# Kernel optimization log

Hardware: AMD Instinct MI355X
Metric: run time of the kernel (lower is better)

## Reference

```python
import jax, jax.numpy as jnp
import numpy as np

B, NQ, NK = 4, 1024, 1536
DQ = DK = DV = 1024
DI = 4096
H = 16
EPS = 1e-5

def _ln(x, g, b):
    mu = jnp.mean(x, axis=-1, keepdims=True)
    var = jnp.mean((x - mu) ** 2, axis=-1, keepdims=True)
    return (x - mu) * jax.lax.rsqrt(var + EPS) * g + b

def setup_inputs() -> dict:
    key = jax.random.key(0)
    ks = jax.random.split(key, 20)
    s = 0.02
    inp = {
        "Q": jax.random.normal(ks[0], (B, NQ, DQ), jnp.float32),
        "K": jax.random.normal(ks[1], (B, NK, DK), jnp.float32),
        "knn_masks": jax.random.normal(ks[2], (B * H, NQ, 1024), jnp.float32),
        "mask_pos": 1024,
        "Wq": jax.random.normal(ks[3], (DQ, DV), jnp.float32) * s,
        "bq": jnp.zeros((DV,), jnp.float32),
        "Wk": jax.random.normal(ks[4], (DK, DV), jnp.float32) * s,
        "bk": jnp.zeros((DV,), jnp.float32),
        "Wv": jax.random.normal(ks[5], (DK, DV), jnp.float32) * s,
        "bv": jnp.zeros((DV,), jnp.float32),
        "Wo0": jax.random.normal(ks[6], (DV, DV), jnp.float32) * s,
        "bo0": jnp.zeros((DV,), jnp.float32),
        "Wo": jax.random.normal(ks[7], (DV, DI), jnp.float32) * s,
        "bo": jnp.zeros((DI,), jnp.float32),
        "Wo2": jax.random.normal(ks[8], (DI, DV), jnp.float32) * s,
        "bo2": jnp.zeros((DV,), jnp.float32),
        "g0": jnp.ones((DV,), jnp.float32),
        "beta0": jnp.zeros((DV,), jnp.float32),
        "g1": jnp.ones((DV,), jnp.float32),
        "beta1": jnp.zeros((DV,), jnp.float32),
    }
    return inp

def reference(Q, K, knn_masks, mask_pos, Wq, bq, Wk, bk, Wv, bv,
              Wo0, bo0, Wo, bo, Wo2, bo2, g0, beta0, g1, beta1):
    dh = DV // H
    q = Q @ Wq + bq                      # [B,NQ,DV]
    k = K @ Wk + bk                      # [B,NK,DV]
    v = K @ Wv + bv
    # torch cat(split(.,dh,2),0) -> head-major [H,B,N,dh]
    qh = q.reshape(B, NQ, H, dh).transpose(2, 0, 1, 3)
    kh = k[:, :mask_pos].reshape(B, mask_pos, H, dh).transpose(2, 0, 1, 3)
    vh = v[:, :mask_pos].reshape(B, mask_pos, H, dh).transpose(2, 0, 1, 3)
    logits = jnp.einsum("hbqd,hbkd->hbqk", qh, kh) / jnp.sqrt(jnp.float32(DV))
    logits = logits + knn_masks.reshape(H, B, NQ, mask_pos)
    attn = jax.nn.softmax(logits, axis=-1)
    o = jnp.einsum("hbqk,hbkd->hbqd", attn, vh)   # [H,B,NQ,dh]
    o = o.transpose(1, 2, 0, 3).reshape(B, NQ, DV)  # concat heads
    o = o @ Wo0 + bo0
    O = q + o
    O = _ln(O, g0, beta0)
    ff = jax.nn.relu(O @ Wo + bo) @ Wo2 + bo2
    O = O + ff
    O = _ln(O, g1, beta1)
    return O
```

## Files before the change

kernel.cpp:

```cpp
#include <hip/hip_runtime.h>
#include <hip/hip_bf16.h>

typedef unsigned short u16;
typedef __attribute__((ext_vector_type(4))) short bf16x4;
typedef __attribute__((ext_vector_type(8))) short bf16x8;
typedef __attribute__((ext_vector_type(4))) float f32x4;

static __device__ __forceinline__ u16 f2b(float f){
  union { float f; unsigned u; } v; v.f = f;
  unsigned r = v.u + 0x7fffu + ((v.u >> 16) & 1u);
  return (u16)(r >> 16);
}
static __device__ __forceinline__ float b2f(u16 h){
  union { unsigned u; float f; } v; v.u = ((unsigned)h) << 16; return v.f;
}
static __device__ __forceinline__ void gld_lds16(const void* g, void* l){
  __builtin_amdgcn_global_load_lds((const __attribute__((address_space(1))) void*)g,
                                   (__attribute__((address_space(3))) void*)l, 16, 0, 0);
}

__global__ __launch_bounds__(256) void prep(const float* __restrict__ Q,
                                            const float* __restrict__ K,
                                            u16* __restrict__ Qb, u16* __restrict__ Kb,
                                            const float* __restrict__ Wq, u16* __restrict__ Wq_t,
                                            const float* __restrict__ Wk, u16* __restrict__ Wk_t,
                                            const float* __restrict__ Wv, u16* __restrict__ Wv_t,
                                            const float* __restrict__ Wo0, u16* __restrict__ Wo0_t,
                                            const float* __restrict__ Wo, u16* __restrict__ Wo_t,
                                            const float* __restrict__ Wo2, u16* __restrict__ Wo2_t){
  __shared__ float tile[64][65];
  const int id = blockIdx.x, t = threadIdx.x;
  if (id < 8192){
    const float* src; u16* dst;
    if (id < 4096){
      src = Q + (size_t)id * 1024; dst = Qb + (size_t)id * 1024;
    } else {
      int r = id - 4096;
      size_t ir = (size_t)r + (size_t)(r >> 10) * 512;
      src = K + ir * 1024; dst = Kb + (size_t)r * 1024;
    }
    const float4 v = *(const float4*)(src + t * 4);
    bf16x4 o;
    o[0] = (short)f2b(v.x); o[1] = (short)f2b(v.y);
    o[2] = (short)f2b(v.z); o[3] = (short)f2b(v.w);
    *(bf16x4*)(dst + t * 4) = o;
    return;
  }
  int wid = id - 8192;
  const float* in; u16* out; int Kd, N, bx, by;
  if (wid < 1024){
    int sel = wid >> 8, local = wid & 255;
    bx = local & 15; by = local >> 4; Kd = 1024; N = 1024;
    in  = (sel == 0) ? Wq   : (sel == 1) ? Wk   : (sel == 2) ? Wv   : Wo0;
    out = (sel == 0) ? Wq_t : (sel == 1) ? Wk_t : (sel == 2) ? Wv_t : Wo0_t;
  } else if (wid < 2048){
    int local = wid - 1024; bx = local & 63; by = local >> 6; Kd = 1024; N = 4096;
    in = Wo; out = Wo_t;
  } else {
    int local = wid - 2048; bx = local & 15; by = local >> 4; Kd = 4096; N = 1024;
    in = Wo2; out = Wo2_t;
  }
  const int k0 = by * 64, n0 = bx * 64;
  const int tr = t >> 4, tc = t & 15;
#pragma unroll
  for (int i = 0; i < 4; i++){
    int r = tr + i * 16;
    float4 v = *(const float4*)(in + (size_t)(k0 + r) * N + n0 + tc * 4);
    tile[r][tc*4+0] = v.x; tile[r][tc*4+1] = v.y; tile[r][tc*4+2] = v.z; tile[r][tc*4+3] = v.w;
  }
  __syncthreads();
#pragma unroll
  for (int i = 0; i < 4; i++){
    int nr = tr + i * 16;
    bf16x4 pk;
#pragma unroll
    for (int j = 0; j < 4; j++) pk[j] = (short)f2b(tile[tc*4+j][nr]);
    *(bf16x4*)(out + (size_t)(n0 + nr) * Kd + k0 + tc * 4) = pk;
  }
}

static __device__ __forceinline__ void gemm_mainloop(const u16* __restrict__ A,
                                                     const u16* __restrict__ Bt,
                                                     int lda, int ldb, int kbeg, int kend,
                                                     int m0, int n0,
                                                     u16* lA, u16* lB, f32x4 acc[4][4]){
  const int t = threadIdx.x, w = t >> 6, l = t & 63;
  const int wr = w >> 1, wc = w & 1;
  const int lrow = l >> 3, lc8 = l & 7;
  const int c = l & 15, g = l >> 4;
  for (int k0 = kbeg; k0 < kend; k0 += 64){
#pragma unroll
    for (int i = 0; i < 4; i++){
      int ch = w * 4 + i;
      int r  = ch * 8 + lrow;
      gld_lds16(A  + (size_t)(m0 + r) * lda + k0 + lc8 * 8, lA + ch * 512);
      gld_lds16(Bt + (size_t)(n0 + r) * ldb + k0 + lc8 * 8, lB + ch * 512);
    }
    __syncthreads();
#pragma unroll
    for (int ks = 0; ks < 2; ks++){
      bf16x8 af[4], bfr[4];
#pragma unroll
      for (int mi = 0; mi < 4; mi++){
        int row = wr * 64 + mi * 16 + c;
        af[mi] = *(const bf16x8*)((const char*)lA + row * 128 + ks * 64 + g * 16);
      }
#pragma unroll
      for (int ni = 0; ni < 4; ni++){
        int row = wc * 64 + ni * 16 + c;
        bfr[ni] = *(const bf16x8*)((const char*)lB + row * 128 + ks * 64 + g * 16);
      }
#pragma unroll
      for (int mi = 0; mi < 4; mi++)
#pragma unroll
        for (int ni = 0; ni < 4; ni++)
          acc[mi][ni] = __builtin_amdgcn_mfma_f32_16x16x32_bf16(af[mi], bfr[ni], acc[mi][ni], 0, 0, 0);
    }
    __syncthreads();
  }
}

__global__ __launch_bounds__(256) void gemm_sk2(const u16* __restrict__ A,
                                                const u16* __restrict__ Bt,
                                                float* __restrict__ pout){
  __shared__ u16 lA[128 * 64];
  __shared__ u16 lB[128 * 64];
  const int t = threadIdx.x, w = t >> 6, l = t & 63;
  const int m0 = blockIdx.y * 128, n0 = blockIdx.x * 128;
  const int wr = w >> 1, wc = w & 1;
  const int c = l & 15, g = l >> 4;
  const int kbeg = blockIdx.z * 512;

  f32x4 acc[4][4];
#pragma unroll
  for (int i = 0; i < 4; i++)
#pragma unroll
    for (int j = 0; j < 4; j++) acc[i][j] = (f32x4){0.f, 0.f, 0.f, 0.f};

  gemm_mainloop(A, Bt, 1024, 1024, kbeg, kbeg + 512, m0, n0, lA, lB, acc);

  float* po = pout + ((size_t)blockIdx.z << 22);
#pragma unroll
  for (int ni = 0; ni < 4; ni++){
    int n = n0 + wc * 64 + ni * 16 + c;
#pragma unroll
    for (int mi = 0; mi < 4; mi++){
      int row0 = m0 + wr * 64 + mi * 16 + 4 * g;
#pragma unroll
      for (int r = 0; r < 4; r++)
        po[(size_t)(row0 + r) * 1024 + n] = acc[mi][ni][r];
    }
  }
}

static __device__ __forceinline__ void loop8p(const u16* __restrict__ A,
                                              const u16* __restrict__ Bt,
                                              int lda, int ldb, int kbeg, int NT,
                                              int m0, int n0,
                                              u16 (*sA)[2][8192], u16 (*sB)[2][8192],
                                              f32x4 acc[8][4]){
  const int t = threadIdx.x, w = t >> 6, l = t & 63;
  const int wr = w >> 2, wc = w & 3;
  const int c = l & 15, g = l >> 4;
  const int sr = t >> 3, scb = (t & 7) << 4;

  auto stA = [&](int d, int h, int T){
#pragma unroll
    for (int i = 0; i < 2; i++){
      int row = i * 64 + sr;
      int Lb  = scb ^ ((row & 7) << 4);
      gld_lds16(A + (size_t)(m0 + h * 128 + row) * lda + kbeg + T * 64 + (Lb >> 1),
                (char*)&sA[d][h][0] + i * 8192 + t * 16);
    }
  };
  auto stB = [&](int d, int h, int T){
#pragma unroll
    for (int i = 0; i < 2; i++){
      int row = i * 64 + sr;
      int Lb  = scb ^ ((row & 7) << 4);
      gld_lds16(Bt + (size_t)(n0 + h * 128 + row) * ldb + kbeg + T * 64 + (Lb >> 1),
                (char*)&sB[d][h][0] + i * 8192 + t * 16);
    }
  };

  stB(0, 0, 0); stB(0, 1, 0); stA(0, 0, 0); stA(0, 1, 0);
  stB(1, 0, 1); stB(1, 1, 1);

  bf16x8 bfr[4][2];
  for (int T = 0; T < NT; ++T){
    const int d = T & 1;
    const char* pa = (const char*)&sA[d][wr][0];
    const char* pb = (const char*)&sB[d][wc >> 1][0];
#pragma unroll
    for (int q = 0; q < 4; ++q){
      if (q == 0){
        if (T + 1 < NT) asm volatile("s_waitcnt vmcnt(4)" ::: "memory");
        else            asm volatile("s_waitcnt vmcnt(0)" ::: "memory");
        asm volatile("" ::: "memory");
        __builtin_amdgcn_s_barrier();
        asm volatile("" ::: "memory");
#pragma unroll
        for (int nf = 0; nf < 4; ++nf){
          int lr = (wc & 1) * 64 + nf * 16 + c;
#pragma unroll
          for (int ks = 0; ks < 2; ++ks)
            bfr[nf][ks] = *(const bf16x8*)(pb + lr * 128 + ((ks * 64 + g * 16) ^ ((lr & 7) << 4)));
        }
      }
      bf16x8 af[2][2];
#pragma unroll
      for (int mi = 0; mi < 2; ++mi){
        int lr = (q * 2 + mi) * 16 + c;
#pragma unroll
        for (int ks = 0; ks < 2; ++ks)
          af[mi][ks] = *(const bf16x8*)(pa + lr * 128 + ((ks * 64 + g * 16) ^ ((lr & 7) << 4)));
      }
      if      (q == 0){ if (T + 1 < NT) stA(d ^ 1, 0, T + 1); }
      else if (q == 1){ if (T + 1 < NT) stA(d ^ 1, 1, T + 1); }
      else if (q == 2){ if (T + 2 < NT) stB(d, 0, T + 2); }
      else            { if (T + 2 < NT) stB(d, 1, T + 2); }
      __builtin_amdgcn_s_setprio(1);
#pragma unroll
      for (int mi = 0; mi < 2; ++mi)
#pragma unroll
        for (int nf = 0; nf < 4; ++nf)
#pragma unroll
          for (int ks = 0; ks < 2; ++ks)
            acc[q * 2 + mi][nf] =
              __builtin_amdgcn_mfma_f32_16x16x32_bf16(af[mi][ks], bfr[nf][ks], acc[q * 2 + mi][nf], 0, 0, 0);
      __builtin_amdgcn_s_setprio(0);
      asm volatile("" ::: "memory");
      __builtin_amdgcn_s_barrier();
      asm volatile("" ::: "memory");
    }
  }
}

template<int EPI>
__global__ __launch_bounds__(512, 2) void gemm8p(const u16* __restrict__ A,
                                                 const u16* __restrict__ Bt,
                                                 const float* __restrict__ bias,
                                                 void* __restrict__ outp,
                                                 int lda, int ldb, int ldout,
                                                 int ksz, int NT){
  __shared__ u16 sA[2][2][8192];
  __shared__ u16 sB[2][2][8192];
  const int t = threadIdx.x, w = t >> 6, l = t & 63;
  const int wr = w >> 2, wc = w & 3;
  const int c = l & 15, g = l >> 4;

  int m0, n0, zidx;
  if (EPI == 0){
    int lid = blockIdx.x + (blockIdx.y << 4);
    int xcd = lid & 7, slot = lid >> 3;
    int bx = ((xcd & 1) << 3) + (slot & 7);
    int by = ((xcd >> 1) << 2) + (slot >> 3);
    m0 = by * 256; n0 = bx * 256; zidx = 0;
  } else {
    int lid = blockIdx.x + (blockIdx.y << 2) + (blockIdx.z << 6);
    int xcd = lid & 7, slot = lid >> 3;
    int bx = slot & 3, rest = slot >> 2;
    int by = (xcd << 1) + (rest & 1);
    zidx = rest >> 1;
    m0 = by * 256; n0 = bx * 256;
  }

  f32x4 acc[8][4];
#pragma unroll
  for (int i = 0; i < 8; i++)
#pragma unroll
    for (int j = 0; j < 4; j++) acc[i][j] = (f32x4){0.f, 0.f, 0.f, 0.f};

  loop8p(A, Bt, lda, ldb, zidx * ksz, NT, m0, n0, sA, sB, acc);

  if (EPI == 0){
    u16* out = (u16*)outp;
#pragma unroll
    for (int nf = 0; nf < 4; ++nf){
      int n = n0 + wc * 64 + nf * 16 + c;
      float bv = bias[n];
#pragma unroll
      for (int mf = 0; mf < 8; ++mf){
        int row0 = m0 + wr * 128 + mf * 16 + 4 * g;
#pragma unroll
        for (int r = 0; r < 4; ++r)
          out[(size_t)(row0 + r) * ldout + n] = f2b(fmaxf(acc[mf][nf][r] + bv, 0.f));
      }
    }
  } else {
    float* po = (float*)outp + ((size_t)zidx << 22);
#pragma unroll
    for (int nf = 0; nf < 4; ++nf){
      int n = n0 + wc * 64 + nf * 16 + c;
#pragma unroll
      for (int mf = 0; mf < 8; ++mf){
        int row0 = m0 + wr * 128 + mf * 16 + 4 * g;
#pragma unroll
        for (int r = 0; r < 4; ++r)
          po[(size_t)(row0 + r) * 1024 + n] = acc[mf][nf][r];
      }
    }
  }
}

__global__ __launch_bounds__(512, 2) void gemm8p_qkv(const u16* __restrict__ Qb,
                                                     const u16* __restrict__ Kb,
                                                     const u16* __restrict__ Wq_t,
                                                     const u16* __restrict__ Wk_t,
                                                     const u16* __restrict__ Wv_t,
                                                     const float* __restrict__ bq,
                                                     const float* __restrict__ bk,
                                                     const float* __restrict__ bv,
                                                     u16* __restrict__ qb,
                                                     u16* __restrict__ kbf,
                                                     u16* __restrict__ vtb){
  __shared__ u16 sA[2][2][8192];
  __shared__ u16 sB[2][2][8192];
  int lid = blockIdx.x + blockIdx.y * 12;
  int xcd = lid & 7, slot = lid >> 3;
  int bx = (xcd & 3) * 3 + slot % 3;
  int by = ((xcd >> 2) << 3) + slot / 3;
  const int sel = bx >> 2;
  const u16* A    = sel ? Kb : Qb;
  const u16* Bt   = (sel == 0) ? Wq_t : (sel == 1) ? Wk_t : Wv_t;
  const float* bi = (sel == 0) ? bq   : (sel == 1) ? bk   : bv;
  const int t = threadIdx.x, w = t >> 6, l = t & 63;
  const int wr = w >> 2, wc = w & 3;
  const int c = l & 15, g = l >> 4;
  const int m0 = by * 256, n0 = (bx & 3) * 256;

  f32x4 acc[8][4];
#pragma unroll
  for (int i = 0; i < 8; i++)
#pragma unroll
    for (int j = 0; j < 4; j++) acc[i][j] = (f32x4){0.f, 0.f, 0.f, 0.f};

  loop8p(A, Bt, 1024, 1024, 0, 16, m0, n0, sA, sB, acc);

  if (sel == 2){
    u16* sl = (w < 4) ? (&sA[0][0][0] + w * 8192) : (&sB[0][0][0] + (w - 4) * 8192);
#pragma unroll
    for (int nf = 0; nf < 4; ++nf){
      int n = n0 + wc * 64 + nf * 16 + c;
      float bv_ = bi[n];
#pragma unroll
      for (int mf = 0; mf < 8; ++mf){
        bf16x4 pk;
#pragma unroll
        for (int r = 0; r < 4; ++r) pk[r] = (short)f2b(acc[mf][nf][r] + bv_);
        *(bf16x4*)(sl + (nf * 16 + c) * 128 + mf * 16 + 4 * g) = pk;
      }
    }
    asm volatile("s_waitcnt lgkmcnt(0)" ::: "memory");
    __builtin_amdgcn_sched_barrier(0);
    const int mg = m0 + wr * 128;
    const int bb = mg >> 10, kb0 = mg & 1023;
    u16* vbase = vtb + ((size_t)bb << 20) + kb0;
#pragma unroll
    for (int j = 0; j < 16; ++j){
      int nl  = (l >> 4) + j * 4;
      int kl  = (l & 15) * 8;
      bf16x8 v = *(const bf16x8*)(sl + nl * 128 + kl);
      *(bf16x8*)(vbase + (size_t)(n0 + wc * 64 + nl) * 1024 + kl) = v;
    }
  } else {
    u16* out = sel ? kbf : qb;
#pragma unroll
    for (int nf = 0; nf < 4; ++nf){
      int n = n0 + wc * 64 + nf * 16 + c;
      float bv_ = bi[n];
#pragma unroll
      for (int mf = 0; mf < 8; ++mf){
        int row0 = m0 + wr * 128 + mf * 16 + 4 * g;
#pragma unroll
        for (int r = 0; r < 4; ++r)
          out[(size_t)(row0 + r) * 1024 + n] = f2b(acc[mf][nf][r] + bv_);
      }
    }
  }
}

__global__ __launch_bounds__(256) void comb_ln0(const float* __restrict__ pp,
                                                const float* __restrict__ bias,
                                                const u16* __restrict__ res,
                                                const float* __restrict__ gw,
                                                const float* __restrict__ bw,
                                                u16* __restrict__ out){
  const int row = blockIdx.x, t = threadIdx.x, w = t >> 6, l = t & 63;
  const size_t i4 = (size_t)row * 1024 + t * 4;
  f32x4 a = *(const f32x4*)(pp + i4);
  f32x4 b = *(const f32x4*)(pp + (1ull << 22) + i4);
  bf16x4 rv = *(const bf16x4*)(res + i4);
  float xs[4], s = 0.f, sq = 0.f;
#pragma unroll
  for (int j = 0; j < 4; j++){
    xs[j] = a[j] + b[j] + bias[t * 4 + j] + b2f((u16)rv[j]);
    s += xs[j]; sq += xs[j] * xs[j];
  }
#pragma unroll
  for (int o = 32; o; o >>= 1){ s += __shfl_xor(s, o); sq += __shfl_xor(sq, o); }
  __shared__ float rs[4], rq[4];
  if (l == 0){ rs[w] = s; rq[w] = sq; }
  __syncthreads();
  s  = rs[0] + rs[1] + rs[2] + rs[3];
  sq = rq[0] + rq[1] + rq[2] + rq[3];
  const float mu   = s * (1.f / 1024.f);
  const float var  = sq * (1.f / 1024.f) - mu * mu;
  const float rstd = rsqrtf(var + 1e-5f);
  bf16x4 o;
#pragma unroll
  for (int j = 0; j < 4; j++) o[j] = (short)f2b((xs[j]-mu)*rstd*gw[t*4+j] + bw[t*4+j]);
  *(bf16x4*)(out + i4) = o;
}

__global__ __launch_bounds__(256) void comb_ln1(const float* __restrict__ pp,
                                                const float* __restrict__ bias,
                                                const u16* __restrict__ res,
                                                const float* __restrict__ gw,
                                                const float* __restrict__ bw,
                                                float* __restrict__ out){
  const int row = blockIdx.x, t = threadIdx.x, w = t >> 6, l = t & 63;
  const size_t i4 = (size_t)row * 1024 + t * 4;
  f32x4 a = *(const f32x4*)(pp + i4);
#pragma unroll
  for (int z = 1; z < 4; z++){
    f32x4 p = *(const f32x4*)(pp + ((size_t)z << 22) + i4);
    a[0] += p[0]; a[1] += p[1]; a[2] += p[2]; a[3] += p[3];
  }
  bf16x4 rv = *(const bf16x4*)(res + i4);
  float xs[4], s = 0.f, sq = 0.f;
#pragma unroll
  for (int j = 0; j < 4; j++){
    xs[j] = a[j] + bias[t * 4 + j] + b2f((u16)rv[j]);
    s += xs[j]; sq += xs[j] * xs[j];
  }
#pragma unroll
  for (int o = 32; o; o >>= 1){ s += __shfl_xor(s, o); sq += __shfl_xor(sq, o); }
  __shared__ float rs[4], rq[4];
  if (l == 0){ rs[w] = s; rq[w] = sq; }
  __syncthreads();
  s  = rs[0] + rs[1] + rs[2] + rs[3];
  sq = rq[0] + rq[1] + rq[2] + rq[3];
  const float mu   = s * (1.f / 1024.f);
  const float var  = sq * (1.f / 1024.f) - mu * mu;
  const float rstd = rsqrtf(var + 1e-5f);
  float4 o4;
  o4.x = (xs[0]-mu)*rstd*gw[t*4+0] + bw[t*4+0];
  o4.y = (xs[1]-mu)*rstd*gw[t*4+1] + bw[t*4+1];
  o4.z = (xs[2]-mu)*rstd*gw[t*4+2] + bw[t*4+2];
  o4.w = (xs[3]-mu)*rstd*gw[t*4+3] + bw[t*4+3];
  *((float4*)out + (size_t)row * 256 + t) = o4;
}

#define ATTN_STEP(IT, CUR, MC) do{                                              \
  if ((IT) < 15) asm volatile("s_waitcnt vmcnt(4)" ::: "memory");               \
  else           asm volatile("s_waitcnt vmcnt(0)" ::: "memory");               \
  __builtin_amdgcn_s_barrier();                                                 \
  asm volatile("" ::: "memory");                                                \
  if ((IT) < 15) stage((CUR) ^ 1, ((IT) + 1) * 64);                             \
  asm volatile("" ::: "memory");                                                \
  const char* kt = (const char*)sK[(CUR)];                                      \
  f32x4 st[4];                                                                  \
  _Pragma("unroll")                                                             \
  for (int nf = 0; nf < 4; nf++){                                               \
    const char* kr = kt + (nf * 16 + c) * 128;                                  \
    bf16x8 ak0 = *(const bf16x8*)(kr + ((g * 16) ^ sw));                        \
    bf16x8 ak1 = *(const bf16x8*)(kr + ((64 + g * 16) ^ sw));                   \
    f32x4 z = (f32x4){0.f, 0.f, 0.f, 0.f};                                      \
    z = __builtin_amdgcn_mfma_f32_16x16x32_bf16(ak0, bq0, z, 0, 0, 0);          \
    z = __builtin_amdgcn_mfma_f32_16x16x32_bf16(ak1, bq1, z, 0, 0, 0);          \
    st[nf] = z;                                                                 \
  }                                                                             \
  float tmax = -INFINITY;                                                       \
  _Pragma("unroll")                                                             \
  for (int nf = 0; nf < 4; nf++)                                                \
    _Pragma("unroll")                                                           \
    for (int r = 0; r < 4; r++){                                                \
      float v = st[nf][r] * 0.03125f + MC[nf][r];                               \
      st[nf][r] = v; tmax = fmaxf(tmax, v);                                     \
    }                                                                           \
  if ((IT) < 14){                                                               \
    _Pragma("unroll")                                                           \
    for (int nf = 0; nf < 4; nf++)                                              \
      MC[nf] = *(const f32x4*)(mbase + ((IT) + 2) * 64 + nf * 16 + g * 4);      \
  }                                                                             \
  tmax = fmaxf(tmax, __shfl_xor(tmax, 16));                                     \
  tmax = fmaxf(tmax, __shfl_xor(tmax, 32));                                     \
  float mnew  = fmaxf(m, tmax);                                                 \
  float alpha = __expf(m - mnew);                                               \
  float rsum = 0.f;                                                             \
  bf16x4 pb[4];                                                                 \
  _Pragma("unroll")                                                             \
  for (int nf = 0; nf < 4; nf++)                                                \
    _Pragma("unroll")                                                           \
    for (int r = 0; r < 4; r++){                                                \
      float p = __expf(st[nf][r] - mnew);                                       \
      rsum += p;                                                                \
      pb[nf][r] = (short)f2b(p);                                                \
    }                                                                           \
  rsum += __shfl_xor(rsum, 16); rsum += __shfl_xor(rsum, 32);                   \
  lsum = lsum * alpha + rsum; m = mnew;                                         \
  _Pragma("unroll")                                                             \
  for (int f = 0; f < 4; f++){                                                  \
    acc[f][0] *= alpha; acc[f][1] *= alpha;                                     \
    acc[f][2] *= alpha; acc[f][3] *= alpha;                                     \
  }                                                                             \
  const char* vtc = (const char*)sV[(CUR)];                                     \
  __builtin_amdgcn_s_setprio(1);                                                \
  _Pragma("unroll")                                                             \
  for (int f = 0; f < 4; f++){                                                  \
    const char* vr = vtc + (f * 16 + c) * 128;                                  \
    _Pragma("unroll")                                                           \
    for (int nf = 0; nf < 4; nf++){                                             \
      bf16x4 av = *(const bf16x4*)(vr + ((nf * 32 + g * 8) ^ sw));              \
      acc[f] = __builtin_amdgcn_mfma_f32_16x16x16bf16_1k(av, pb[nf], acc[f], 0, 0, 0); \
    }                                                                           \
  }                                                                             \
  __builtin_amdgcn_s_setprio(0);                                                \
}while(0)

__global__ __launch_bounds__(256, 4) void attn_k(const u16* __restrict__ qb,
                                                 const u16* __restrict__ kb,
                                                 const u16* __restrict__ vt,
                                                 const float* __restrict__ mask,
                                                 u16* __restrict__ ob){
  __shared__ u16 sK[2][4096];
  __shared__ u16 sV[2][4096];

  const int t = threadIdx.x, w = t >> 6, l = t & 63;
  const int c = l & 15, g = l >> 4;
  const int lid  = blockIdx.x + (blockIdx.y << 4) + (blockIdx.z << 8);
  const int xcd  = lid & 7, slot = lid >> 3;
  const int grp  = xcd + ((slot >> 4) << 3);
  const int q0   = (slot & 15) * 64;
  const int h    = grp & 15, b = grp >> 4;
  const int qrow = q0 + w * 16 + c;
  const size_t qoff = ((size_t)(b * 1024 + qrow)) * 1024 + h * 64;
  const bf16x8 bq0 = *(const bf16x8*)(qb + qoff + g * 8);
  const bf16x8 bq1 = *(const bf16x8*)(qb + qoff + 32 + g * 8);
  const u16* kbase = kb + ((size_t)b * 1024) * 1024 + h * 64;
  const u16* vbase = vt + ((size_t)b << 20) + (size_t)(h * 64) * 1024;
  const float* mbase = mask + ((size_t)(h * 4 + b) * 1024 + qrow) * 1024;

  const int lr3 = l >> 3, lc3 = l & 7;
  const int ch0 = w * 2;

  auto stage = [&](int buf, int kv){
#pragma unroll
    for (int i = 0; i < 2; i++){
      int ch  = ch0 + i;
      int row = ch * 8 + lr3;
      int L   = (lc3 * 16) ^ ((row & 7) << 4);
      gld_lds16(kbase + (size_t)(kv + row) * 1024 + (L >> 1), &sK[buf][ch * 512]);
      gld_lds16(vbase + (size_t)row * 1024 + kv + (L >> 1),   &sV[buf][ch * 512]);
    }
  };

  float m = -INFINITY, lsum = 0.f;
  f32x4 acc[4];
#pragma unroll
  for (int f = 0; f < 4; f++) acc[f] = (f32x4){0.f, 0.f, 0.f, 0.f};

  stage(0, 0);
  asm volatile("" ::: "memory");
  f32x4 mA[4], mB[4];
#pragma unroll
  for (int nf = 0; nf < 4; nf++) mA[nf] = *(const f32x4*)(mbase + nf * 16 + g * 4);
  asm volatile("" ::: "memory");
#pragma unroll
  for (int nf = 0; nf < 4; nf++) mB[nf] = *(const f32x4*)(mbase + 64 + nf * 16 + g * 4);

  const int sw = (c & 7) << 4;
  for (int ii = 0; ii < 8; ++ii){
    ATTN_STEP(2 * ii,     0, mA);
    ATTN_STEP(2 * ii + 1, 1, mB);
  }

  const float inv = 1.f / lsum;
  u16* sO = &sK[0][0];
#pragma unroll
  for (int f = 0; f < 4; f++){
    bf16x4 pk;
#pragma unroll
    for (int r = 0; r < 4; r++) pk[r] = (short)f2b(acc[f][r] * inv);
    *(bf16x4*)(sO + (w * 16 + c) * 64 + f * 16 + 4 * g) = pk;
  }
  asm volatile("s_waitcnt lgkmcnt(0)" ::: "memory");
  __builtin_amdgcn_sched_barrier(0);
  {
    int rl  = w * 16 + (l >> 2);
    int d0  = (l & 3) * 16;
    bf16x8 v0 = *(const bf16x8*)(sO + rl * 64 + d0);
    bf16x8 v1 = *(const bf16x8*)(sO + rl * 64 + d0 + 8);
    u16* dst = ob + ((size_t)(b * 1024 + q0 + rl)) * 1024 + h * 64 + d0;
    *(bf16x8*)(dst)     = v0;
    *(bf16x8*)(dst + 8) = v1;
  }
}

extern "C" void kernel_launch(void* const* d_in, const int* in_sizes, int n_in,
                              void* d_out, int out_size, void* d_ws, size_t ws_size,
                              hipStream_t stream){
  const float* Q    = (const float*)d_in[0];
  const float* K    = (const float*)d_in[1];
  const float* mask = (const float*)d_in[2];
  const float* Wq   = (const float*)d_in[4];  const float* bq  = (const float*)d_in[5];
  const float* Wk   = (const float*)d_in[6];  const float* bk  = (const float*)d_in[7];
  const float* Wv   = (const float*)d_in[8];  const float* bv  = (const float*)d_in[9];
  const float* Wo0  = (const float*)d_in[10]; const float* bo0 = (const float*)d_in[11];
  const float* Wo   = (const float*)d_in[12]; const float* bo  = (const float*)d_in[13];
  const float* Wo2  = (const float*)d_in[14]; const float* bo2 = (const float*)d_in[15];
  const float* g0   = (const float*)d_in[16]; const float* be0 = (const float*)d_in[17];
  const float* g1   = (const float*)d_in[18]; const float* be1 = (const float*)d_in[19];

  uint8_t* W = (uint8_t*)d_ws;
  const size_t MB = 1024ull * 1024ull;
  u16* Wq_t  = (u16*)(W + 0);
  u16* Wk_t  = (u16*)(W + 2  * MB);
  u16* Wv_t  = (u16*)(W + 4  * MB);
  u16* Wo0_t = (u16*)(W + 6  * MB);
  u16* Wo_t  = (u16*)(W + 8  * MB);
  u16* Wo2_t = (u16*)(W + 16 * MB);
  u16* Qb    = (u16*)(W + 24 * MB);
  u16* Kb    = (u16*)(W + 32 * MB);
  u16* qb    = (u16*)(W + 40 * MB);
  u16* kbf   = (u16*)(W + 48 * MB);
  u16* vtb   = (u16*)(W + 56 * MB);
  u16* ob    = (u16*)(W + 24 * MB);
  u16* x1b   = (u16*)(W + 64 * MB);
  u16* hb    = (u16*)(W + 32 * MB);
  float* pp  = (float*)(W + 72 * MB);

  prep<<<11264, 256, 0, stream>>>(Q, K, Qb, Kb, Wq, Wq_t, Wk, Wk_t, Wv, Wv_t,
                                  Wo0, Wo0_t, Wo, Wo_t, Wo2, Wo2_t);

  gemm8p_qkv<<<dim3(12, 16), 512, 0, stream>>>(Qb, Kb, Wq_t, Wk_t, Wv_t,
                                               bq, bk, bv, qb, kbf, vtb);

  attn_k<<<dim3(16, 16, 4), 256, 0, stream>>>(qb, kbf, vtb, mask, ob);

  gemm_sk2<<<dim3(8, 32, 2), 256, 0, stream>>>(ob, Wo0_t, pp);
  comb_ln0<<<4096, 256, 0, stream>>>(pp, bo0, qb, g0, be0, x1b);

  gemm8p<0><<<dim3(16, 16), 512, 0, stream>>>(x1b, Wo_t, bo, hb, 1024, 1024, 4096, 0, 16);
  gemm8p<1><<<dim3(4, 16, 4), 512, 0, stream>>>(hb, Wo2_t, nullptr, pp, 4096, 4096, 1024, 1024, 16);
  comb_ln1<<<4096, 256, 0, stream>>>(pp, bo2, x1b, g1, be1, (float*)d_out);
}
```

Before: 299.0 us.

## Store split-K partials in bf16 and route Wo0 GEMM through gemm8p

The split-K partial outputs of the output-projection GEMMs are now written in bf16 instead of fp32, which halves partial-buffer write and read traffic in the GEMM epilogue and in the combine+layernorm kernels. The Wo0 projection moves from the simpler 128x128 gemm_sk2 kernel to the pipelined 256x256 gemm8p kernel with 4-way split-K, and the two layernorm combine kernels are merged into one templated kernel. Rounding partial sums to bf16 before the final reduction adds some precision loss.

```diff
diff --git a/kernel.cpp b/kernel.cpp
--- a/kernel.cpp
+++ b/kernel.cpp
@@ -79,80 +79,6 @@
   }
 }
 
-static __device__ __forceinline__ void gemm_mainloop(const u16* __restrict__ A,
-                                                     const u16* __restrict__ Bt,
-                                                     int lda, int ldb, int kbeg, int kend,
-                                                     int m0, int n0,
-                                                     u16* lA, u16* lB, f32x4 acc[4][4]){
-  const int t = threadIdx.x, w = t >> 6, l = t & 63;
-  const int wr = w >> 1, wc = w & 1;
-  const int lrow = l >> 3, lc8 = l & 7;
-  const int c = l & 15, g = l >> 4;
-  for (int k0 = kbeg; k0 < kend; k0 += 64){
-#pragma unroll
-    for (int i = 0; i < 4; i++){
-      int ch = w * 4 + i;
-      int r  = ch * 8 + lrow;
-      gld_lds16(A  + (size_t)(m0 + r) * lda + k0 + lc8 * 8, lA + ch * 512);
-      gld_lds16(Bt + (size_t)(n0 + r) * ldb + k0 + lc8 * 8, lB + ch * 512);
-    }
-    __syncthreads();
-#pragma unroll
-    for (int ks = 0; ks < 2; ks++){
-      bf16x8 af[4], bfr[4];
-#pragma unroll
-      for (int mi = 0; mi < 4; mi++){
-        int row = wr * 64 + mi * 16 + c;
-        af[mi] = *(const bf16x8*)((const char*)lA + row * 128 + ks * 64 + g * 16);
-      }
-#pragma unroll
-      for (int ni = 0; ni < 4; ni++){
-        int row = wc * 64 + ni * 16 + c;
-        bfr[ni] = *(const bf16x8*)((const char*)lB + row * 128 + ks * 64 + g * 16);
-      }
-#pragma unroll
-      for (int mi = 0; mi < 4; mi++)
-#pragma unroll
-        for (int ni = 0; ni < 4; ni++)
-          acc[mi][ni] = __builtin_amdgcn_mfma_f32_16x16x32_bf16(af[mi], bfr[ni], acc[mi][ni], 0, 0, 0);
-    }
-    __syncthreads();
-  }
-}
-
-__global__ __launch_bounds__(256) void gemm_sk2(const u16* __restrict__ A,
-                                                const u16* __restrict__ Bt,
-                                                float* __restrict__ pout){
-  __shared__ u16 lA[128 * 64];
-  __shared__ u16 lB[128 * 64];
-  const int t = threadIdx.x, w = t >> 6, l = t & 63;
-  const int m0 = blockIdx.y * 128, n0 = blockIdx.x * 128;
-  const int wr = w >> 1, wc = w & 1;
-  const int c = l & 15, g = l >> 4;
-  const int kbeg = blockIdx.z * 512;
-
-  f32x4 acc[4][4];
-#pragma unroll
-  for (int i = 0; i < 4; i++)
-#pragma unroll
-    for (int j = 0; j < 4; j++) acc[i][j] = (f32x4){0.f, 0.f, 0.f, 0.f};
-
-  gemm_mainloop(A, Bt, 1024, 1024, kbeg, kbeg + 512, m0, n0, lA, lB, acc);
-
-  float* po = pout + ((size_t)blockIdx.z << 22);
-#pragma unroll
-  for (int ni = 0; ni < 4; ni++){
-    int n = n0 + wc * 64 + ni * 16 + c;
-#pragma unroll
-    for (int mi = 0; mi < 4; mi++){
-      int row0 = m0 + wr * 64 + mi * 16 + 4 * g;
-#pragma unroll
-      for (int r = 0; r < 4; r++)
-        po[(size_t)(row0 + r) * 1024 + n] = acc[mi][ni][r];
-    }
-  }
-}
-
 static __device__ __forceinline__ void loop8p(const u16* __restrict__ A,
                                               const u16* __restrict__ Bt,
                                               int lda, int ldb, int kbeg, int NT,
@@ -288,7 +214,7 @@
       }
     }
   } else {
-    float* po = (float*)outp + ((size_t)zidx << 22);
+    u16* po = (u16*)outp + (size_t)zidx * (4096ull * 1024ull);
 #pragma unroll
     for (int nf = 0; nf < 4; ++nf){
       int n = n0 + wc * 64 + nf * 16 + c;
@@ -297,7 +223,7 @@
         int row0 = m0 + wr * 128 + mf * 16 + 4 * g;
 #pragma unroll
         for (int r = 0; r < 4; ++r)
-          po[(size_t)(row0 + r) * 1024 + n] = acc[mf][nf][r];
+          po[(size_t)(row0 + r) * 1024 + n] = f2b(acc[mf][nf][r]);
       }
     }
   }
@@ -380,23 +306,28 @@
   }
 }
 
-__global__ __launch_bounds__(256) void comb_ln0(const float* __restrict__ pp,
-                                                const float* __restrict__ bias,
-                                                const u16* __restrict__ res,
-                                                const float* __restrict__ gw,
-                                                const float* __restrict__ bw,
-                                                u16* __restrict__ out){
+template<int NP, int F32OUT>
+__global__ __launch_bounds__(256) void comb_ln(const u16* __restrict__ pp,
+                                               const float* __restrict__ bias,
+                                               const u16* __restrict__ res,
+                                               const float* __restrict__ gw,
+                                               const float* __restrict__ bw,
+                                               void* __restrict__ outp){
   const int row = blockIdx.x, t = threadIdx.x, w = t >> 6, l = t & 63;
   const size_t i4 = (size_t)row * 1024 + t * 4;
-  f32x4 a = *(const f32x4*)(pp + i4);
-  f32x4 b = *(const f32x4*)(pp + (1ull << 22) + i4);
   bf16x4 rv = *(const bf16x4*)(res + i4);
-  float xs[4], s = 0.f, sq = 0.f;
-#pragma unroll
-  for (int j = 0; j < 4; j++){
-    xs[j] = a[j] + b[j] + bias[t * 4 + j] + b2f((u16)rv[j]);
-    s += xs[j]; sq += xs[j] * xs[j];
-  }
+  float xs[4];
+#pragma unroll
+  for (int j = 0; j < 4; j++) xs[j] = bias[t * 4 + j] + b2f((u16)rv[j]);
+#pragma unroll
+  for (int z = 0; z < NP; z++){
+    bf16x4 p = *(const bf16x4*)(pp + (size_t)z * (4096ull * 1024ull) + i4);
+#pragma unroll
+    for (int j = 0; j < 4; j++) xs[j] += b2f((u16)p[j]);
+  }
+  float s = 0.f, sq = 0.f;
+#pragma unroll
+  for (int j = 0; j < 4; j++){ s += xs[j]; sq += xs[j] * xs[j]; }
 #pragma unroll
   for (int o = 32; o; o >>= 1){ s += __shfl_xor(s, o); sq += __shfl_xor(sq, o); }
   __shared__ float rs[4], rq[4];
@@ -407,49 +338,19 @@
   const float mu   = s * (1.f / 1024.f);
   const float var  = sq * (1.f / 1024.f) - mu * mu;
   const float rstd = rsqrtf(var + 1e-5f);
-  bf16x4 o;
-#pragma unroll
-  for (int j = 0; j < 4; j++) o[j] = (short)f2b((xs[j]-mu)*rstd*gw[t*4+j] + bw[t*4+j]);
-  *(bf16x4*)(out + i4) = o;
-}
-
-__global__ __launch_bounds__(256) void comb_ln1(const float* __restrict__ pp,
-                                                const float* __restrict__ bias,
-                                                const u16* __restrict__ res,
-                                                const float* __restrict__ gw,
-                                                const float* __restrict__ bw,
-                                                float* __restrict__ out){
-  const int row = blockIdx.x, t = threadIdx.x, w = t >> 6, l = t & 63;
-  const size_t i4 = (size_t)row * 1024 + t * 4;
-  f32x4 a = *(const f32x4*)(pp + i4);
-#pragma unroll
-  for (int z = 1; z < 4; z++){
-    f32x4 p = *(const f32x4*)(pp + ((size_t)z << 22) + i4);
-    a[0] += p[0]; a[1] += p[1]; a[2] += p[2]; a[3] += p[3];
-  }
-  bf16x4 rv = *(const bf16x4*)(res + i4);
-  float xs[4], s = 0.f, sq = 0.f;
-#pragma unroll
-  for (int j = 0; j < 4; j++){
-    xs[j] = a[j] + bias[t * 4 + j] + b2f((u16)rv[j]);
-    s += xs[j]; sq += xs[j] * xs[j];
-  }
-#pragma unroll
-  for (int o = 32; o; o >>= 1){ s += __shfl_xor(s, o); sq += __shfl_xor(sq, o); }
-  __shared__ float rs[4], rq[4];
-  if (l == 0){ rs[w] = s; rq[w] = sq; }
-  __syncthreads();
-  s  = rs[0] + rs[1] + rs[2] + rs[3];
-  sq = rq[0] + rq[1] + rq[2] + rq[3];
-  const float mu   = s * (1.f / 1024.f);
-  const float var  = sq * (1.f / 1024.f) - mu * mu;
-  const float rstd = rsqrtf(var + 1e-5f);
-  float4 o4;
-  o4.x = (xs[0]-mu)*rstd*gw[t*4+0] + bw[t*4+0];
-  o4.y = (xs[1]-mu)*rstd*gw[t*4+1] + bw[t*4+1];
-  o4.z = (xs[2]-mu)*rstd*gw[t*4+2] + bw[t*4+2];
-  o4.w = (xs[3]-mu)*rstd*gw[t*4+3] + bw[t*4+3];
-  *((float4*)out + (size_t)row * 256 + t) = o4;
+  if (F32OUT){
+    float4 o4;
+    o4.x = (xs[0]-mu)*rstd*gw[t*4+0] + bw[t*4+0];
+    o4.y = (xs[1]-mu)*rstd*gw[t*4+1] + bw[t*4+1];
+    o4.z = (xs[2]-mu)*rstd*gw[t*4+2] + bw[t*4+2];
+    o4.w = (xs[3]-mu)*rstd*gw[t*4+3] + bw[t*4+3];
+    *((float4*)outp + (size_t)row * 256 + t) = o4;
+  } else {
+    bf16x4 o;
+#pragma unroll
+    for (int j = 0; j < 4; j++) o[j] = (short)f2b((xs[j]-mu)*rstd*gw[t*4+j] + bw[t*4+j]);
+    *((bf16x4*)outp + (size_t)row * 256 + t) = o;
+  }
 }
 
 #define ATTN_STEP(IT, CUR, MC) do{                                              \
@@ -629,7 +530,7 @@
   u16* ob    = (u16*)(W + 24 * MB);
   u16* x1b   = (u16*)(W + 64 * MB);
   u16* hb    = (u16*)(W + 32 * MB);
-  float* pp  = (float*)(W + 72 * MB);
+  u16* ppb   = (u16*)(W + 72 * MB);
 
   prep<<<11264, 256, 0, stream>>>(Q, K, Qb, Kb, Wq, Wq_t, Wk, Wk_t, Wv, Wv_t,
                                   Wo0, Wo0_t, Wo, Wo_t, Wo2, Wo2_t);
@@ -639,10 +540,10 @@
 
   attn_k<<<dim3(16, 16, 4), 256, 0, stream>>>(qb, kbf, vtb, mask, ob);
 
-  gemm_sk2<<<dim3(8, 32, 2), 256, 0, stream>>>(ob, Wo0_t, pp);
-  comb_ln0<<<4096, 256, 0, stream>>>(pp, bo0, qb, g0, be0, x1b);
+  gemm8p<1><<<dim3(4, 16, 4), 512, 0, stream>>>(ob, Wo0_t, nullptr, ppb, 1024, 1024, 1024, 256, 4);
+  comb_ln<4, 0><<<4096, 256, 0, stream>>>(ppb, bo0, qb, g0, be0, x1b);
 
   gemm8p<0><<<dim3(16, 16), 512, 0, stream>>>(x1b, Wo_t, bo, hb, 1024, 1024, 4096, 0, 16);
-  gemm8p<1><<<dim3(4, 16, 4), 512, 0, stream>>>(hb, Wo2_t, nullptr, pp, 4096, 4096, 1024, 1024, 16);
-  comb_ln1<<<4096, 256, 0, stream>>>(pp, bo2, x1b, g1, be1, (float*)d_out);
-}
+  gemm8p<1><<<dim3(4, 16, 4), 512, 0, stream>>>(hb, Wo2_t, nullptr, ppb, 4096, 4096, 1024, 1024, 16);
+  comb_ln<4, 1><<<4096, 256, 0, stream>>>(ppb, bo2, x1b, g1, be1, d_out);
+}
```

After: 295.2 us. About the same (-1.3%).
